# Optimization experiments

Hardware: AMD Instinct MI355X
Metric: run time of the kernel (lower is better)

Reference implementation:

```python
import jax, jax.numpy as jnp
import numpy as np

D_K = 64
D_MODEL = 1024
SEQ = 4096
BATCH = 4


def setup_inputs() -> dict:
    key = jax.random.key(0)
    ks = jax.random.split(key, 7)
    s = 1.0 / np.sqrt(D_MODEL)
    return {
        "x": jax.random.normal(ks[0], (BATCH, SEQ, D_MODEL), dtype=jnp.float32),
        "wq": jax.random.uniform(ks[1], (D_K, D_MODEL), jnp.float32, -s, s),
        "bq": jax.random.uniform(ks[2], (D_K,), jnp.float32, -s, s),
        "wk": jax.random.uniform(ks[3], (D_K, D_MODEL), jnp.float32, -s, s),
        "bk": jax.random.uniform(ks[4], (D_K,), jnp.float32, -s, s),
        "wv": jax.random.uniform(ks[5], (D_K, D_MODEL), jnp.float32, -s, s),
        "bv": jax.random.uniform(ks[6], (D_K,), jnp.float32, -s, s),
    }


def reference(x, wq, bq, wk, bk, wv, bv):
    # q,k,v: [B,T,d_k]
    q = jnp.einsum('btc,dc->btd', x, wq) + bq
    k = jnp.einsum('btc,dc->btd', x, wk) + bk
    v = jnp.einsum('btc,dc->btd', x, wv) + bv
    scale = 1.0 / np.sqrt(D_K).astype(np.float32)
    scores = jnp.einsum('bqd,bkd->bqk', q, k) * scale  # [B,T,T]
    T = x.shape[1]
    causal = jnp.tril(jnp.ones((T, T), dtype=bool))
    scores = jnp.where(causal, scores, -jnp.inf)
    sm = jax.nn.softmax(scores, axis=-1)
    return jnp.einsum('bqk,bkd->bqd', sm, v)
```

## Files before the change

kernel.cpp:

```cpp
#include <hip/hip_runtime.h>

typedef __attribute__((ext_vector_type(8))) short short8;
typedef __attribute__((ext_vector_type(4))) short short4v;
typedef __attribute__((ext_vector_type(4))) float f32x4;

#define D_KV   64
#define SEQ    4096
#define NBATCH 4
#define DMODEL 1024

static __device__ __forceinline__ unsigned short f32_to_bf16(float f) {
  unsigned u = __builtin_bit_cast(unsigned, f);
  u = (u + 0x7FFFu + ((u >> 16) & 1u)) >> 16;
  return (unsigned short)u;
}

__global__ __launch_bounds__(256) void wcvt_kernel(
    const float* __restrict__ wq, const float* __restrict__ wk,
    const float* __restrict__ wv, unsigned short* __restrict__ wfrag) {
  const int fid = blockIdx.x * 256 + threadIdx.x;
  const int nt = fid >> 11, ks = (fid >> 6) & 31, lane = fid & 63;
  const int l16 = lane & 15, lq = lane >> 4;
  const float* w = (nt < 4) ? wq : (nt < 8) ? wk : wv;
  const float* src = w + ((nt & 3) * 16 + l16) * DMODEL + ks * 32 + lq * 8;
  short8 v;
#pragma unroll
  for (int j = 0; j < 8; ++j) v[j] = (short)f32_to_bf16(src[j]);
  *reinterpret_cast<short8*>(wfrag + (long)fid * 8) = v;
}

__global__ __launch_bounds__(256) void qkv_proj_kernel(
    const float* __restrict__ x, const unsigned short* __restrict__ wfrag,
    const float* __restrict__ bq, const float* __restrict__ bk,
    const float* __restrict__ bv,
    unsigned short* __restrict__ Qf, unsigned short* __restrict__ Kf,
    unsigned short* __restrict__ Vf) {
  __shared__ __align__(16) unsigned short lds_x[16 * 64];
  const int tid = threadIdx.x, lane = tid & 63, wave = tid >> 6;
  const int l16 = lane & 15, lq = lane >> 4;
  const long rowbase = (long)blockIdx.x * 16;

  const int srow = tid >> 4, sq = tid & 15;
  const float* sgptr = x + (rowbase + srow) * DMODEL + sq * 4;
  const int swz_w = srow * 128 + ((sq * 8) ^ ((srow & 7) << 4));
  unsigned char* lx = (unsigned char*)lds_x;

  f32x4 acc[3];
#pragma unroll
  for (int i = 0; i < 3; ++i) acc[i] = (f32x4){0.f, 0.f, 0.f, 0.f};

  const unsigned short* wbase = wfrag + (long)(3 * wave) * 16384 + lane * 8;

  for (int s = 0; s < 16; ++s) {
    const f32x4 xv = *reinterpret_cast<const f32x4*>(sgptr + s * 64);
    short8 wv[3][2];
#pragma unroll
    for (int i = 0; i < 3; ++i)
#pragma unroll
      for (int kc = 0; kc < 2; ++kc)
        wv[i][kc] = *reinterpret_cast<const short8*>(
            wbase + (long)i * 16384 + (2 * s + kc) * 512);
    __syncthreads();
    short4v xs;
#pragma unroll
    for (int j = 0; j < 4; ++j) xs[j] = (short)f32_to_bf16(xv[j]);
    *reinterpret_cast<short4v*>(lx + swz_w) = xs;
    __syncthreads();
    short8 a[2];
#pragma unroll
    for (int kc = 0; kc < 2; ++kc)
      a[kc] = *reinterpret_cast<const short8*>(
          lx + l16 * 128 + (((kc * 4 + lq) ^ (l16 & 7)) << 4));
#pragma unroll
    for (int i = 0; i < 3; ++i)
#pragma unroll
      for (int kc = 0; kc < 2; ++kc)
        acc[i] = __builtin_amdgcn_mfma_f32_16x16x32_bf16(a[kc], wv[i][kc],
                                                         acc[i], 0, 0, 0);
  }

#pragma unroll
  for (int i = 0; i < 3; ++i) {
    const int nt = 3 * wave + i;
    const int mat = nt >> 2;
    const int dcol = ((nt & 3) << 4) | l16;
    const float bias = (mat == 0 ? bq : mat == 1 ? bk : bv)[dcol];
    const int c = dcol >> 5, lqp = (dcol >> 3) & 3, jj = dcol & 7;
#pragma unroll
    for (int r = 0; r < 4; ++r) {
      const long t = rowbase + lq * 4 + r;
      const float sum = acc[i][r] + bias;
      if (mat == 0) {
        Qf[(((t >> 4) * 2 + c) * 64 + lqp * 16 + (t & 15)) * 8 + jj] =
            f32_to_bf16(sum * 0.125f);
      } else if (mat == 1) {
        Kf[((((t >> 6) * 4 + ((t >> 4) & 3)) * 2 + c) * 64 + lqp * 16 +
            (t & 15)) * 8 + jj] = f32_to_bf16(sum);
      } else {
        Vf[((((t >> 6) * 4 + (dcol >> 4)) * 2 + ((t >> 5) & 1)) * 64 +
            ((t >> 3) & 3) * 16 + (dcol & 15)) * 8 + (t & 7)] =
            f32_to_bf16(sum);
      }
    }
  }
}

__global__ __launch_bounds__(256) void attn_kernel(
    const unsigned short* __restrict__ Qf, const unsigned short* __restrict__ Kf,
    const unsigned short* __restrict__ Vf, float* __restrict__ out) {
  __shared__ __align__(16) unsigned short p_lds[4][16][72];
  __shared__ __align__(16) float lds_o[4][16][68];
  __shared__ float lds_ml[4][16][2];
  __shared__ float lds_gl[16];

  const int tid = threadIdx.x;
  const int lane = tid & 63;
  const int wave = tid >> 6;
  const int l16 = lane & 15, lq = lane >> 4;
  const int b = blockIdx.y;
  const int tile = 255 - blockIdx.x;
  const int qbase = tile * 16;
  const long qrow = (long)b * SEQ + qbase;

  short8 qf[2];
#pragma unroll
  for (int c = 0; c < 2; ++c)
    qf[c] = *reinterpret_cast<const short8*>(
        Qf + ((qrow >> 4) * 2 + c) * 512 + lane * 8);

  f32x4 o[4];
#pragma unroll
  for (int dt = 0; dt < 4; ++dt) o[dt] = (f32x4){0.f, 0.f, 0.f, 0.f};
  float m = -INFINITY, ell = 0.f;

  const long ktile0 = (long)b * 64;
  const int nkv = qbase / 64 + 1;
  for (int kt = wave; kt < nkv; kt += 4) {
    const int kvbase = kt * 64;
    const unsigned short* kb = Kf + (ktile0 + kt) * 4096 + lane * 8;
    const unsigned short* vb = Vf + (ktile0 + kt) * 4096 + lane * 8;
    f32x4 s[4];
#pragma unroll
    for (int ct = 0; ct < 4; ++ct) s[ct] = (f32x4){0.f, 0.f, 0.f, 0.f};
#pragma unroll
    for (int ct = 0; ct < 4; ++ct)
#pragma unroll
      for (int c = 0; c < 2; ++c) {
        short8 kf = *reinterpret_cast<const short8*>(kb + (ct * 2 + c) * 512);
        s[ct] = __builtin_amdgcn_mfma_f32_16x16x32_bf16(kf, qf[c], s[ct], 0, 0, 0);
      }
    if (kt == nkv - 1) {
      const int qg = qbase + l16;
#pragma unroll
      for (int ct = 0; ct < 4; ++ct)
#pragma unroll
        for (int r = 0; r < 4; ++r)
          if (kvbase + ct * 16 + lq * 4 + r > qg) s[ct][r] = -INFINITY;
    }
    float mx = -INFINITY;
#pragma unroll
    for (int ct = 0; ct < 4; ++ct)
#pragma unroll
      for (int r = 0; r < 4; ++r) mx = fmaxf(mx, s[ct][r]);
    mx = fmaxf(mx, __shfl_xor(mx, 16, 64));
    mx = fmaxf(mx, __shfl_xor(mx, 32, 64));
    const float nm = fmaxf(m, mx);
    const float alpha = __expf(m - nm);
    float rs = 0.f;
#pragma unroll
    for (int ct = 0; ct < 4; ++ct)
#pragma unroll
      for (int r = 0; r < 4; ++r) {
        const float p = __expf(s[ct][r] - nm);
        s[ct][r] = p;
        rs += p;
      }
    rs += __shfl_xor(rs, 16, 64);
    rs += __shfl_xor(rs, 32, 64);
    ell = ell * alpha + rs;
    m = nm;
#pragma unroll
    for (int dt = 0; dt < 4; ++dt) o[dt] *= alpha;
#pragma unroll
    for (int ct = 0; ct < 4; ++ct)
#pragma unroll
      for (int r = 0; r < 4; ++r)
        p_lds[wave][l16][ct * 16 + lq * 4 + r] = f32_to_bf16(s[ct][r]);
    short8 pf[2];
#pragma unroll
    for (int c = 0; c < 2; ++c)
      pf[c] = *reinterpret_cast<const short8*>(&p_lds[wave][l16][c * 32 + lq * 8]);
#pragma unroll
    for (int dt = 0; dt < 4; ++dt)
#pragma unroll
      for (int c = 0; c < 2; ++c) {
        short8 vf = *reinterpret_cast<const short8*>(vb + (dt * 2 + c) * 512);
        o[dt] = __builtin_amdgcn_mfma_f32_16x16x32_bf16(vf, pf[c], o[dt], 0, 0, 0);
      }
  }

  if (lane < 16) {
    lds_ml[wave][l16][0] = m;
    lds_ml[wave][l16][1] = ell;
  }
  __syncthreads();
  const float m0 = lds_ml[0][l16][0], m1 = lds_ml[1][l16][0];
  const float m2 = lds_ml[2][l16][0], m3 = lds_ml[3][l16][0];
  const float g = fmaxf(fmaxf(m0, m1), fmaxf(m2, m3));
  const float gl = lds_ml[0][l16][1] * __expf(m0 - g) +
                   lds_ml[1][l16][1] * __expf(m1 - g) +
                   lds_ml[2][l16][1] * __expf(m2 - g) +
                   lds_ml[3][l16][1] * __expf(m3 - g);
  const float myscale = __expf(m - g);
  if (wave == 0 && lane < 16) lds_gl[l16] = gl;
#pragma unroll
  for (int dt = 0; dt < 4; ++dt)
#pragma unroll
    for (int r = 0; r < 4; ++r)
      lds_o[wave][l16][dt * 16 + lq * 4 + r] = o[dt][r] * myscale;
  __syncthreads();
#pragma unroll
  for (int j = 0; j < 4; ++j) {
    const int e = tid + 256 * j;
    const int row = e >> 6, col = e & 63;
    const float sum = lds_o[0][row][col] + lds_o[1][row][col] +
                      lds_o[2][row][col] + lds_o[3][row][col];
    out[(qrow + row) * D_KV + col] = sum / lds_gl[row];
  }
}

extern "C" void kernel_launch(void* const* d_in, const int* in_sizes, int n_in,
                              void* d_out, int out_size, void* d_ws, size_t ws_size,
                              hipStream_t stream) {
  const float* x  = (const float*)d_in[0];
  const float* wq = (const float*)d_in[1];
  const float* bq = (const float*)d_in[2];
  const float* wk = (const float*)d_in[3];
  const float* bk = (const float*)d_in[4];
  const float* wv = (const float*)d_in[5];
  const float* bv = (const float*)d_in[6];
  float* out = (float*)d_out;

  unsigned short* ws    = (unsigned short*)d_ws;
  unsigned short* wfrag = ws;
  unsigned short* Qf    = ws + 196608;
  unsigned short* Kf    = Qf + 1048576;
  unsigned short* Vf    = Kf + 1048576;

  wcvt_kernel<<<96, 256, 0, stream>>>(wq, wk, wv, wfrag);
  qkv_proj_kernel<<<1024, 256, 0, stream>>>(x, wfrag, bq, bk, bv, Qf, Kf, Vf);
  dim3 ag(256, NBATCH);
  attn_kernel<<<ag, 256, 0, stream>>>(Qf, Kf, Vf, out);
}
```

Baseline: 62.59 us.

## Stage full 16-row x tile in LDS once before QKV projection MFMA loop

```diff
diff --git a/kernel.cpp b/kernel.cpp
--- a/kernel.cpp
+++ b/kernel.cpp
@@ -35,48 +35,42 @@
     const float* __restrict__ bv,
     unsigned short* __restrict__ Qf, unsigned short* __restrict__ Kf,
     unsigned short* __restrict__ Vf) {
-  __shared__ __align__(16) unsigned short lds_x[16 * 64];
+  __shared__ __align__(16) unsigned short lds_x[16 * 1024];
   const int tid = threadIdx.x, lane = tid & 63, wave = tid >> 6;
   const int l16 = lane & 15, lq = lane >> 4;
   const long rowbase = (long)blockIdx.x * 16;
 
   const int srow = tid >> 4, sq = tid & 15;
   const float* sgptr = x + (rowbase + srow) * DMODEL + sq * 4;
-  const int swz_w = srow * 128 + ((sq * 8) ^ ((srow & 7) << 4));
   unsigned char* lx = (unsigned char*)lds_x;
-
-  f32x4 acc[3];
-#pragma unroll
-  for (int i = 0; i < 3; ++i) acc[i] = (f32x4){0.f, 0.f, 0.f, 0.f};
-
-  const unsigned short* wbase = wfrag + (long)(3 * wave) * 16384 + lane * 8;
-
+#pragma unroll
   for (int s = 0; s < 16; ++s) {
     const f32x4 xv = *reinterpret_cast<const f32x4*>(sgptr + s * 64);
-    short8 wv[3][2];
-#pragma unroll
-    for (int i = 0; i < 3; ++i)
-#pragma unroll
-      for (int kc = 0; kc < 2; ++kc)
-        wv[i][kc] = *reinterpret_cast<const short8*>(
-            wbase + (long)i * 16384 + (2 * s + kc) * 512);
-    __syncthreads();
     short4v xs;
 #pragma unroll
     for (int j = 0; j < 4; ++j) xs[j] = (short)f32_to_bf16(xv[j]);
-    *reinterpret_cast<short4v*>(lx + swz_w) = xs;
-    __syncthreads();
-    short8 a[2];
-#pragma unroll
-    for (int kc = 0; kc < 2; ++kc)
-      a[kc] = *reinterpret_cast<const short8*>(
-          lx + l16 * 128 + (((kc * 4 + lq) ^ (l16 & 7)) << 4));
-#pragma unroll
-    for (int i = 0; i < 3; ++i)
-#pragma unroll
-      for (int kc = 0; kc < 2; ++kc)
-        acc[i] = __builtin_amdgcn_mfma_f32_16x16x32_bf16(a[kc], wv[i][kc],
-                                                         acc[i], 0, 0, 0);
+    const int woff = srow * 2048 + ((sq * 8 + s * 128) ^ ((srow & 7) << 4));
+    *reinterpret_cast<short4v*>(lx + woff) = xs;
+  }
+  __syncthreads();
+
+  f32x4 acc[3];
+#pragma unroll
+  for (int i = 0; i < 3; ++i) acc[i] = (f32x4){0.f, 0.f, 0.f, 0.f};
+
+  const unsigned short* wbase = wfrag + (long)(3 * wave) * 16384 + lane * 8;
+  const unsigned char* lrow = lx + l16 * 2048;
+
+#pragma unroll 8
+  for (int ks = 0; ks < 32; ++ks) {
+    const short8 a = *reinterpret_cast<const short8*>(
+        lrow + ((ks * 64 + lq * 16) ^ ((l16 & 7) << 4)));
+#pragma unroll
+    for (int i = 0; i < 3; ++i) {
+      const short8 b = *reinterpret_cast<const short8*>(
+          wbase + (long)i * 16384 + ks * 512);
+      acc[i] = __builtin_amdgcn_mfma_f32_16x16x32_bf16(a, b, acc[i], 0, 0, 0);
+    }
   }
 
 #pragma unroll
```

After: 68.46 us. +9.4%, slower.
